# Performance work log

Measured on AMD Instinct MI355X. Metric: run time of the kernel, lower is better.

## Reference

```python
import jax, jax.numpy as jnp
import numpy as np
import math

B, S, D, H = 4, 2048, 1024, 16
DK = D // H

def setup_inputs() -> dict:
    key = jax.random.key(0)
    ks = jax.random.split(key, 6)
    scale = 1.0 / math.sqrt(D)
    x = jax.random.normal(ks[0], (B, S, D), dtype=jnp.float32)
    mask = jnp.tril(jnp.ones((S, S), dtype=jnp.int32))[None, None]  # [1,1,S,S] causal
    Wq = jax.random.normal(ks[1], (D, D), dtype=jnp.float32) * scale
    Wk = jax.random.normal(ks[2], (D, D), dtype=jnp.float32) * scale
    Wv = jax.random.normal(ks[3], (D, D), dtype=jnp.float32) * scale
    Wo = jax.random.normal(ks[4], (D, D), dtype=jnp.float32) * scale
    z = jnp.zeros((D,), dtype=jnp.float32)
    return {"x": x, "mask": mask, "Wq": Wq, "bq": z, "Wk": Wk, "bk": z,
            "Wv": Wv, "bv": z, "Wo": Wo, "bo": z}

def reference(x, mask, Wq, bq, Wk, bk, Wv, bv, Wo, bo):
    bsz, seq_len, d_model = x.shape
    def split_heads(t):  # [B,S,D] -> [B,H,S,DK]
        return t.reshape(bsz, seq_len, H, DK).transpose(0, 2, 1, 3)
    Q = split_heads(x @ Wq + bq)
    K = split_heads(x @ Wk + bk)
    V = split_heads(x @ Wv + bv)
    scores = jnp.einsum('bhqd,bhkd->bhqk', Q, K) / jnp.sqrt(jnp.asarray(DK, x.dtype))
    scores = jnp.where(mask == 0, jnp.asarray(-jnp.inf, x.dtype), scores)
    attn = jax.nn.softmax(scores, axis=-1)
    # dropout is identity in eval mode
    context = jnp.einsum('bhqk,bhkd->bhqd', attn, V)
    context = context.transpose(0, 2, 1, 3).reshape(bsz, seq_len, d_model)
    return context @ Wo + bo
```

## Files before the change

### kernel.cpp

```cpp
#include <hip/hip_runtime.h>
#include <hip/hip_bf16.h>
#include <math.h>

#define BATCH 4
#define SEQ   2048
#define DMODEL 1024
#define NHEAD 16
#define DHEAD 64
#define MROWS (BATCH * SEQ)
#define SC_Q  0.1803368801111244f

typedef __attribute__((ext_vector_type(8))) short short8;
typedef __attribute__((ext_vector_type(4))) float f32x4;
typedef __attribute__((ext_vector_type(4))) unsigned short ushort4v;

__device__ inline unsigned short f2bf(float f) {
    union { float f; unsigned int u; } v; v.f = f;
    unsigned int r = v.u + 0x7FFFu + ((v.u >> 16) & 1u);
    return (unsigned short)(r >> 16);
}

__device__ inline unsigned int cvt_pk_bf16(float a, float b) {
    unsigned int r;
    asm("v_cvt_pk_bf16_f32 %0, %1, %2" : "=v"(r) : "v"(a), "v"(b));
    return r;
}

__device__ __forceinline__ void g2l16(const unsigned short* g, unsigned short* l) {
    __builtin_amdgcn_global_load_lds(
        (const __attribute__((address_space(1))) unsigned int*)g,
        (__attribute__((address_space(3))) unsigned int*)l, 16, 0, 0);
}

#define SBAR()  do { __builtin_amdgcn_s_barrier(); asm volatile("" ::: "memory"); } while (0)

__global__ __launch_bounds__(256) void cvt_bf16_kernel(
    const float* __restrict__ src, unsigned short* __restrict__ dst, int n4)
{
    const int i = blockIdx.x * 256 + threadIdx.x;
    if (i < n4) {
        float4 v = ((const float4*)src)[i];
        ushort4v o = { f2bf(v.x), f2bf(v.y), f2bf(v.z), f2bf(v.w) };
        ((ushort4v*)dst)[i] = o;
    }
}

__global__ __launch_bounds__(256) void bias_pack_kernel(
    const float* __restrict__ bq, const float* __restrict__ bk,
    const float* __restrict__ bv, float* __restrict__ b3)
{
    const int i = blockIdx.x * 256 + threadIdx.x;
    if (i < DMODEL) {
        b3[i]              = bq[i];
        b3[i + DMODEL]     = bk[i];
        b3[i + 2 * DMODEL] = bv[i];
    }
}

__global__ __launch_bounds__(256) void transpose_cvt_kernel(
    const float* __restrict__ W0, const float* __restrict__ W1,
    const float* __restrict__ W2, const float* __restrict__ W3,
    unsigned short* __restrict__ T0, unsigned short* __restrict__ T1,
    unsigned short* __restrict__ T2, unsigned short* __restrict__ T3)
{
    const float* W; unsigned short* T;
    switch (blockIdx.z) {
        case 0: W = W0; T = T0; break;
        case 1: W = W1; T = T1; break;
        case 2: W = W2; T = T2; break;
        default: W = W3; T = T3; break;
    }
    __shared__ float tile[32][33];
    const int r0 = blockIdx.y * 32, c0 = blockIdx.x * 32;
    const int c = threadIdx.x & 31, r = threadIdx.x >> 5;
    #pragma unroll
    for (int i = 0; i < 4; ++i)
        tile[r + i * 8][c] = W[(size_t)(r0 + r + i * 8) * DMODEL + c0 + c];
    __syncthreads();
    #pragma unroll
    for (int i = 0; i < 4; ++i)
        T[(size_t)(c0 + r + i * 8) * DMODEL + r0 + c] = f2bf(tile[c][r + i * 8]);
}

__global__ __launch_bounds__(256) void transpose_v_kernel(
    const unsigned short* __restrict__ Vin, unsigned short* __restrict__ Vt)
{
    __shared__ unsigned short t[64][72];
    const int tid = threadIdx.x;
    const int kt = blockIdx.x, bh = blockIdx.y;
    const unsigned short* src = Vin + ((size_t)bh * SEQ + kt * 64) * DHEAD;
    const int r = tid >> 3, c = (tid & 7) * 8;
    *(short8*)&t[r][c]      = *(const short8*)(src + (size_t)r * DHEAD + c);
    *(short8*)&t[r + 32][c] = *(const short8*)(src + (size_t)(r + 32) * DHEAD + c);
    __syncthreads();
    unsigned short* dst = Vt + (size_t)bh * DHEAD * SEQ + kt * 64;
    const int d = tid >> 3, p0 = (tid & 7) * 8;
    short8 v0, v1;
    #pragma unroll
    for (int i = 0; i < 8; ++i) {
        const int p = p0 + i;
        const int k = (p & 32) | (((p >> 2) & 1) << 4) | (((p >> 3) & 3) << 2) | (p & 3);
        v0[i] = (short)t[k][d];
        v1[i] = (short)t[k][d + 32];
    }
    *(short8*)(dst + (size_t)d * SEQ + p0)        = v0;
    *(short8*)(dst + (size_t)(d + 32) * SEQ + p0) = v1;
}

__device__ __forceinline__ void gemm_main_8ph(
    const unsigned short* __restrict__ A, const unsigned short* __restrict__ Bt,
    f32x4 (&acc)[4][4], int m0, int n0, int wm, int wn, int l15, int quad)
{
    __shared__ unsigned short As[3][256 * 64];
    __shared__ unsigned short Bs[3][128 * 64];

    const int tid = threadIdx.x;

    #pragma unroll
    for (int i = 0; i < 4; ++i)
        #pragma unroll
        for (int j = 0; j < 4; ++j) acc[i][j] = (f32x4){0.f, 0.f, 0.f, 0.f};

    const unsigned short* gA[4];
    const unsigned short* gB[2];
    int cA[4], cB[2];
    #pragma unroll
    for (int j = 0; j < 4; ++j) {
        const int c = tid + j * 512, row = c >> 3, gq = (c & 7) ^ (row & 7);
        gA[j] = A + (size_t)(m0 + row) * DMODEL + gq * 8;
        cA[j] = c * 8;
    }
    #pragma unroll
    for (int j = 0; j < 2; ++j) {
        const int c = tid + j * 512, row = c >> 3, gq = (c & 7) ^ (row & 7);
        gB[j] = Bt + (size_t)(n0 + row) * DMODEL + gq * 8;
        cB[j] = c * 8;
    }

    #pragma unroll
    for (int tt = 0; tt < 2; ++tt) {
        #pragma unroll
        for (int j = 0; j < 4; ++j) { g2l16(gA[j], &As[tt][cA[j]]); gA[j] += 64; }
        #pragma unroll
        for (int j = 0; j < 2; ++j) { g2l16(gB[j], &Bs[tt][cB[j]]); gB[j] += 64; }
    }
    asm volatile("s_waitcnt vmcnt(6)" ::: "memory");
    SBAR();

    const int rm[4] = { wm + l15, wm + 16 + l15, wm + 32 + l15, wm + 48 + l15 };
    const int rn[4] = { wn + l15, wn + 16 + l15, wn + 32 + l15, wn + 48 + l15 };

    int cur = 0, sb = 2;
    #pragma unroll 1
    for (int t = 0; t < DMODEL / 64; ++t) {
        const unsigned short* As_c = &As[cur][0];
        const unsigned short* Bs_c = &Bs[cur][0];
        unsigned short* As_s = &As[sb][0];
        unsigned short* Bs_s = &Bs[sb][0];
        const bool st = (t < DMODEL / 64 - 2);

        short8 af[4], bfr[4];

        #pragma unroll
        for (int i = 0; i < 4; ++i) {
            af[i]  = *(const short8*)&As_c[rm[i] * 64 + (quad ^ (rm[i] & 7)) * 8];
            bfr[i] = *(const short8*)&Bs_c[rn[i] * 64 + (quad ^ (rn[i] & 7)) * 8];
        }
        if (st) { g2l16(gA[0], &As_s[cA[0]]); gA[0] += 64;
                  g2l16(gA[1], &As_s[cA[1]]); gA[1] += 64;
                  g2l16(gA[2], &As_s[cA[2]]); gA[2] += 64; }
        SBAR();
        __builtin_amdgcn_s_setprio(1);
        #pragma unroll
        for (int mi = 0; mi < 4; ++mi)
            #pragma unroll
            for (int ni = 0; ni < 4; ++ni)
                acc[mi][ni] = __builtin_amdgcn_mfma_f32_16x16x32_bf16(
                    af[mi], bfr[ni], acc[mi][ni], 0, 0, 0);
        __builtin_amdgcn_s_setprio(0);
        SBAR();

        #pragma unroll
        for (int i = 0; i < 4; ++i) {
            af[i]  = *(const short8*)&As_c[rm[i] * 64 + ((4 + quad) ^ (rm[i] & 7)) * 8];
            bfr[i] = *(const short8*)&Bs_c[rn[i] * 64 + ((4 + quad) ^ (rn[i] & 7)) * 8];
        }
        if (st) { g2l16(gA[3], &As_s[cA[3]]); gA[3] += 64;
                  g2l16(gB[0], &Bs_s[cB[0]]); gB[0] += 64;
                  g2l16(gB[1], &Bs_s[cB[1]]); gB[1] += 64; }
        if (st)
            asm volatile("s_waitcnt vmcnt(6)" ::: "memory");
        else if (t == DMODEL / 64 - 2)
            asm volatile("s_waitcnt vmcnt(0)" ::: "memory");
        SBAR();
        __builtin_amdgcn_s_setprio(1);
        #pragma unroll
        for (int mi = 0; mi < 4; ++mi)
            #pragma unroll
            for (int ni = 0; ni < 4; ++ni)
                acc[mi][ni] = __builtin_amdgcn_mfma_f32_16x16x32_bf16(
                    af[mi], bfr[ni], acc[mi][ni], 0, 0, 0);
        __builtin_amdgcn_s_setprio(0);
        SBAR();

        cur = (cur == 2) ? 0 : cur + 1;
        sb  = (sb  == 2) ? 0 : sb  + 1;
    }
}

__global__ __launch_bounds__(512, 2) void gemm_qkv(
    const unsigned short* __restrict__ A, const unsigned short* __restrict__ Bt,
    const float* __restrict__ bias3, unsigned short* __restrict__ QKV )
{
    const int tid  = threadIdx.x;
    const int wave = tid >> 6, lane = tid & 63;
    const int l15  = lane & 15, quad = lane >> 4;
    const int wm   = (wave >> 1) * 64;
    const int wn   = (wave & 1) * 64;
    const int m0   = blockIdx.y * 256;
    const int n0   = blockIdx.x * 128;

    f32x4 acc[4][4];
    gemm_main_8ph(A, Bt, acc, m0, n0, wm, wn, l15, quad);

    const size_t elems = (size_t)MROWS * DMODEL;
    #pragma unroll
    for (int mi = 0; mi < 4; ++mi) {
        #pragma unroll
        for (int r = 0; r < 4; ++r) {
            const int m = m0 + wm + mi * 16 + quad * 4 + r;
            const int b = m >> 11, s = m & 2047;
            #pragma unroll
            for (int ni = 0; ni < 4; ++ni) {
                const int n   = n0 + wn + ni * 16 + l15;
                const int seg = n >> 10, nn = n & 1023;
                const int h = nn >> 6, dk = nn & 63;
                const float sc  = (seg == 0) ? SC_Q : 1.0f;
                const float val = (acc[mi][ni][r] + bias3[n]) * sc;
                QKV[seg * elems + (((size_t)(b * NHEAD + h)) * SEQ + s) * DHEAD + dk] = f2bf(val);
            }
        }
    }
}

__global__ __launch_bounds__(512, 2) void gemm_out(
    const unsigned short* __restrict__ A, const unsigned short* __restrict__ Bt,
    const float* __restrict__ bias, float* __restrict__ Cout)
{
    const int tid  = threadIdx.x;
    const int wave = tid >> 6, lane = tid & 63;
    const int l15  = lane & 15, quad = lane >> 4;
    const int wm   = (wave >> 1) * 64;
    const int wn   = (wave & 1) * 64;
    const int m0   = blockIdx.y * 256;
    const int n0   = blockIdx.x * 128;

    f32x4 acc[4][4];
    gemm_main_8ph(A, Bt, acc, m0, n0, wm, wn, l15, quad);

    #pragma unroll
    for (int mi = 0; mi < 4; ++mi) {
        #pragma unroll
        for (int r = 0; r < 4; ++r) {
            const int m = m0 + wm + mi * 16 + quad * 4 + r;
            #pragma unroll
            for (int ni = 0; ni < 4; ++ni) {
                const int n = n0 + wn + ni * 16 + l15;
                Cout[(size_t)m * DMODEL + n] = acc[mi][ni][r] + bias[n];
            }
        }
    }
}

__global__ __launch_bounds__(256, 4) void attn_mfma7(
    const unsigned short* __restrict__ Q, const unsigned short* __restrict__ K,
    const unsigned short* __restrict__ VtG, unsigned short* __restrict__ ctx_out)
{
    __shared__ alignas(16) unsigned short Ks[2][64 * 64];
    __shared__ alignas(16) unsigned short Vs[2][64 * 64];

    const int tid  = threadIdx.x;
    const int wave = tid >> 6, lane = tid & 63;
    const int l15  = lane & 15, quad = lane >> 4;
    const int qa   = blockIdx.x;
    const int qb   = 31 - qa;
    const int bh   = blockIdx.y;
    const int b    = bh >> 4, h = bh & 15;

    const unsigned short* Kb0 = K   + (size_t)bh * SEQ * DHEAD;
    const unsigned short* Vb0 = VtG + (size_t)bh * DHEAD * SEQ;

    short8 qf[2][2];
    #pragma unroll
    for (int g = 0; g < 2; ++g) {
        const int qtile = g ? qb : qa;
        const unsigned short* qrow =
            Q + ((size_t)bh * SEQ + qtile * 64 + wave * 16 + l15) * DHEAD + quad * 8;
        qf[g][0] = *(const short8*)qrow;
        qf[g][1] = *(const short8*)(qrow + 32);
    }

    f32x4 Of[2][4];
    float lsum[2] = {0.f, 0.f};
    #pragma unroll
    for (int g = 0; g < 2; ++g)
        #pragma unroll
        for (int i = 0; i < 4; ++i) Of[g][i] = (f32x4){0.f, 0.f, 0.f, 0.f};

    const int qloc = wave * 16 + l15;
    const f32x4 zero4 = (f32x4){0.f, 0.f, 0.f, 0.f};

    const int ck0 = tid >> 3, cg0 = tid & 7;
    const int ck1 = (tid + 256) >> 3, cg1 = tid & 7;

    #define STAGE(buf, jb)                                                          \
        do {                                                                        \
            const unsigned short* Kt_ = Kb0 + (size_t)(jb) * 64 * DHEAD;            \
            const unsigned short* Vt_ = Vb0 + (jb) * 64;                            \
            g2l16(Kt_ + (size_t)ck0 * DHEAD + (cg0 ^ (ck0 & 7)) * 8,                \
                  &Ks[buf][(tid) * 8]);                                             \
            g2l16(Vt_ + (size_t)ck0 * SEQ   + (cg0 ^ (ck0 & 7)) * 8,                \
                  &Vs[buf][(tid) * 8]);                                             \
            g2l16(Kt_ + (size_t)ck1 * DHEAD + (cg1 ^ (ck1 & 7)) * 8,                \
                  &Ks[buf][(tid + 256) * 8]);                                       \
            g2l16(Vt_ + (size_t)ck1 * SEQ   + (cg1 ^ (ck1 & 7)) * 8,                \
                  &Vs[buf][(tid + 256) * 8]);                                       \
        } while (0)

    STAGE(0, 0);

    for (int jb = 0; jb <= qb; ++jb) {
        const int cur = jb & 1;
        asm volatile("s_waitcnt vmcnt(0)" ::: "memory");
        __syncthreads();
        if (jb < qb) STAGE(cur ^ 1, jb + 1);

        const bool act0  = (jb <= qa);
        const bool diag0 = (jb == qa);
        const bool diag1 = (jb == qb);
        const unsigned short* KsC = &Ks[cur][0];
        const unsigned short* VsC = &Vs[cur][0];

        union { unsigned int u[4]; short8 v; } pa[2][2];
        #pragma unroll
        for (int nt = 0; nt < 4; ++nt) {
            const int k = nt * 16 + l15;
            const short8 a0 = *(const short8*)&KsC[(k * 8 + ( quad      ^ (k & 7))) * 8];
            const short8 a1 = *(const short8*)&KsC[(k * 8 + ((quad + 4) ^ (k & 7))) * 8];

            f32x4 s1 = __builtin_amdgcn_mfma_f32_16x16x32_bf16(a0, qf[1][0], zero4, 0, 0, 0);
            s1       = __builtin_amdgcn_mfma_f32_16x16x32_bf16(a1, qf[1][1], s1,    0, 0, 0);
            f32x4 p1;
            #pragma unroll
            for (int r = 0; r < 4; ++r) p1[r] = __builtin_amdgcn_exp2f(s1[r]);
            if (diag1) {
                #pragma unroll
                for (int r = 0; r < 4; ++r)
                    if (nt * 16 + quad * 4 + r > qloc) p1[r] = 0.f;
            }
            lsum[1] += (p1[0] + p1[1]) + (p1[2] + p1[3]);
            pa[1][nt >> 1].u[(nt & 1) * 2]     = cvt_pk_bf16(p1[0], p1[1]);
            pa[1][nt >> 1].u[(nt & 1) * 2 + 1] = cvt_pk_bf16(p1[2], p1[3]);

            if (act0) {
                f32x4 s0 = __builtin_amdgcn_mfma_f32_16x16x32_bf16(a0, qf[0][0], zero4, 0, 0, 0);
                s0       = __builtin_amdgcn_mfma_f32_16x16x32_bf16(a1, qf[0][1], s0,    0, 0, 0);
                f32x4 p0;
                #pragma unroll
                for (int r = 0; r < 4; ++r) p0[r] = __builtin_amdgcn_exp2f(s0[r]);
                if (diag0) {
                    #pragma unroll
                    for (int r = 0; r < 4; ++r)
                        if (nt * 16 + quad * 4 + r > qloc) p0[r] = 0.f;
                }
                lsum[0] += (p0[0] + p0[1]) + (p0[2] + p0[3]);
                pa[0][nt >> 1].u[(nt & 1) * 2]     = cvt_pk_bf16(p0[0], p0[1]);
                pa[0][nt >> 1].u[(nt & 1) * 2 + 1] = cvt_pk_bf16(p0[2], p0[3]);
            }
        }

        #pragma unroll
        for (int cc = 0; cc < 2; ++cc) {
            #pragma unroll
            for (int nt = 0; nt < 4; ++nt) {
                const int d = nt * 16 + l15;
                const short8 vb = *(const short8*)
                    &VsC[(d * 8 + ((cc * 4 + quad) ^ (d & 7))) * 8];
                Of[1][nt] = __builtin_amdgcn_mfma_f32_16x16x32_bf16(
                    pa[1][cc].v, vb, Of[1][nt], 0, 0, 0);
                if (act0)
                    Of[0][nt] = __builtin_amdgcn_mfma_f32_16x16x32_bf16(
                        pa[0][cc].v, vb, Of[0][nt], 0, 0, 0);
            }
        }
    }
    #undef STAGE

    #pragma unroll
    for (int g = 0; g < 2; ++g) {
        const int qtile = g ? qb : qa;
        float l = lsum[g];
        l += __shfl_xor(l, 16);
        l += __shfl_xor(l, 32);
        #pragma unroll
        for (int r = 0; r < 4; ++r) {
            const float inv = 1.0f / __shfl(l, quad * 4 + r);
            const int s = qtile * 64 + wave * 16 + quad * 4 + r;
            unsigned short* o = ctx_out + ((size_t)(b * SEQ + s)) * DMODEL + h * DHEAD;
            #pragma unroll
            for (int nt = 0; nt < 4; ++nt)
                o[nt * 16 + l15] = f2bf(Of[g][nt][r] * inv);
        }
    }
}

extern "C" void kernel_launch(void* const* d_in, const int* in_sizes, int n_in,
                              void* d_out, int out_size, void* d_ws, size_t ws_size,
                              hipStream_t stream) {
    const float* x  = (const float*)d_in[0];
    const float* Wq = (const float*)d_in[2];
    const float* bq = (const float*)d_in[3];
    const float* Wk = (const float*)d_in[4];
    const float* bk = (const float*)d_in[5];
    const float* Wv = (const float*)d_in[6];
    const float* bv = (const float*)d_in[7];
    const float* Wo = (const float*)d_in[8];
    const float* bo = (const float*)d_in[9];
    float* out = (float*)d_out;

    const size_t elems  = (size_t)MROWS * DMODEL;
    const size_t welems = (size_t)DMODEL * DMODEL;
    unsigned short* xbf   = (unsigned short*)d_ws;
    unsigned short* WqkvT = xbf + elems;
    unsigned short* WoT   = WqkvT + 3 * welems;
    unsigned short* Qbuf  = WoT + welems;
    unsigned short* Kbuf  = Qbuf + elems;
    unsigned short* Vbuf  = Kbuf + elems;
    unsigned short* VtG   = Vbuf + elems;
    unsigned short* Cbuf  = VtG + elems;
    float*          bias3 = (float*)(Cbuf + elems);

    dim3 blk(256);
    dim3 blk2(512);

    cvt_bf16_kernel<<<dim3((int)(elems / 4 / 256)), blk, 0, stream>>>(x, xbf, (int)(elems / 4));
    transpose_cvt_kernel<<<dim3(32, 32, 4), blk, 0, stream>>>(
        Wq, Wk, Wv, Wo, WqkvT, WqkvT + welems, WqkvT + 2 * welems, WoT);
    bias_pack_kernel<<<dim3(4), blk, 0, stream>>>(bq, bk, bv, bias3);

    dim3 gqkv(3 * DMODEL / 128, MROWS / 256);
    gemm_qkv<<<gqkv, blk2, 0, stream>>>(xbf, WqkvT, bias3, Qbuf);

    transpose_v_kernel<<<dim3(SEQ / 64, BATCH * NHEAD), blk, 0, stream>>>(Vbuf, VtG);

    dim3 gattn(16, BATCH * NHEAD);
    attn_mfma7<<<gattn, blk, 0, stream>>>(Qbuf, Kbuf, VtG, Cbuf);

    dim3 gout(DMODEL / 128, MROWS / 256);
    gemm_out<<<gout, blk2, 0, stream>>>(Cbuf, WoT, bo, out);
}
```

Before: 275.9 us.

## Merge prep kernels into one launch and add wave priority hints in attention

The three preprocessing kernels (x bf16 conversion, weight transpose-convert, bias packing) become one launch that dispatches on block index, removing two kernel launches and the gaps between them. In the attention loop, s_setprio raises wave priority around the MFMA/exp sections, and __syncthreads is replaced by a raw s_barrier with a compiler memory fence. The merged kernel has divergent block roles and a shared-memory tile that only the transpose branch uses. The priority hints may or may not improve interleaving between the waves on a SIMD.

```diff
diff --git a/kernel.cpp b/kernel.cpp
--- a/kernel.cpp
+++ b/kernel.cpp
@@ -34,52 +34,51 @@
 
 #define SBAR()  do { __builtin_amdgcn_s_barrier(); asm volatile("" ::: "memory"); } while (0)
 
-__global__ __launch_bounds__(256) void cvt_bf16_kernel(
-    const float* __restrict__ src, unsigned short* __restrict__ dst, int n4)
-{
-    const int i = blockIdx.x * 256 + threadIdx.x;
-    if (i < n4) {
-        float4 v = ((const float4*)src)[i];
-        ushort4v o = { f2bf(v.x), f2bf(v.y), f2bf(v.z), f2bf(v.w) };
-        ((ushort4v*)dst)[i] = o;
-    }
-}
-
-__global__ __launch_bounds__(256) void bias_pack_kernel(
-    const float* __restrict__ bq, const float* __restrict__ bk,
-    const float* __restrict__ bv, float* __restrict__ b3)
-{
-    const int i = blockIdx.x * 256 + threadIdx.x;
-    if (i < DMODEL) {
-        b3[i]              = bq[i];
-        b3[i + DMODEL]     = bk[i];
-        b3[i + 2 * DMODEL] = bv[i];
-    }
-}
-
-__global__ __launch_bounds__(256) void transpose_cvt_kernel(
+__global__ __launch_bounds__(256) void prep_kernel(
+    const float* __restrict__ x, unsigned short* __restrict__ xbf,
     const float* __restrict__ W0, const float* __restrict__ W1,
     const float* __restrict__ W2, const float* __restrict__ W3,
     unsigned short* __restrict__ T0, unsigned short* __restrict__ T1,
-    unsigned short* __restrict__ T2, unsigned short* __restrict__ T3)
-{
-    const float* W; unsigned short* T;
-    switch (blockIdx.z) {
-        case 0: W = W0; T = T0; break;
-        case 1: W = W1; T = T1; break;
-        case 2: W = W2; T = T2; break;
-        default: W = W3; T = T3; break;
-    }
+    unsigned short* __restrict__ T2, unsigned short* __restrict__ T3,
+    const float* __restrict__ bq, const float* __restrict__ bk,
+    const float* __restrict__ bv, float* __restrict__ b3)
+{
     __shared__ float tile[32][33];
-    const int r0 = blockIdx.y * 32, c0 = blockIdx.x * 32;
-    const int c = threadIdx.x & 31, r = threadIdx.x >> 5;
-    #pragma unroll
-    for (int i = 0; i < 4; ++i)
-        tile[r + i * 8][c] = W[(size_t)(r0 + r + i * 8) * DMODEL + c0 + c];
-    __syncthreads();
-    #pragma unroll
-    for (int i = 0; i < 4; ++i)
-        T[(size_t)(c0 + r + i * 8) * DMODEL + r0 + c] = f2bf(tile[c][r + i * 8]);
+    const int bid = blockIdx.x, tid = threadIdx.x;
+
+    if (bid < 8192) {
+        const int i = bid * 256 + tid;
+        float4 v = ((const float4*)x)[i];
+        ushort4v o = { f2bf(v.x), f2bf(v.y), f2bf(v.z), f2bf(v.w) };
+        ((ushort4v*)xbf)[i] = o;
+    } else if (bid < 12288) {
+        const int t = bid - 8192;
+        const int z = t >> 10, rem = t & 1023;
+        const int by = rem >> 5, bx = rem & 31;
+        const float* W; unsigned short* T;
+        switch (z) {
+            case 0: W = W0; T = T0; break;
+            case 1: W = W1; T = T1; break;
+            case 2: W = W2; T = T2; break;
+            default: W = W3; T = T3; break;
+        }
+        const int r0 = by * 32, c0 = bx * 32;
+        const int c = tid & 31, r = tid >> 5;
+        #pragma unroll
+        for (int i = 0; i < 4; ++i)
+            tile[r + i * 8][c] = W[(size_t)(r0 + r + i * 8) * DMODEL + c0 + c];
+        __syncthreads();
+        #pragma unroll
+        for (int i = 0; i < 4; ++i)
+            T[(size_t)(c0 + r + i * 8) * DMODEL + r0 + c] = f2bf(tile[c][r + i * 8]);
+    } else {
+        const int i = (bid - 12288) * 256 + tid;
+        if (i < DMODEL) {
+            b3[i]              = bq[i];
+            b3[i + DMODEL]     = bk[i];
+            b3[i + 2 * DMODEL] = bv[i];
+        }
+    }
 }
 
 __global__ __launch_bounds__(256) void transpose_v_kernel(
@@ -272,7 +271,7 @@
     }
 }
 
-__global__ __launch_bounds__(256, 4) void attn_mfma7(
+__global__ __launch_bounds__(256, 4) void attn_mfma8(
     const unsigned short* __restrict__ Q, const unsigned short* __restrict__ K,
     const unsigned short* __restrict__ VtG, unsigned short* __restrict__ ctx_out)
 {
@@ -332,7 +331,7 @@
     for (int jb = 0; jb <= qb; ++jb) {
         const int cur = jb & 1;
         asm volatile("s_waitcnt vmcnt(0)" ::: "memory");
-        __syncthreads();
+        SBAR();
         if (jb < qb) STAGE(cur ^ 1, jb + 1);
 
         const bool act0  = (jb <= qa);
@@ -342,6 +341,7 @@
         const unsigned short* VsC = &Vs[cur][0];
 
         union { unsigned int u[4]; short8 v; } pa[2][2];
+        __builtin_amdgcn_s_setprio(1);
         #pragma unroll
         for (int nt = 0; nt < 4; ++nt) {
             const int k = nt * 16 + l15;
@@ -378,7 +378,9 @@
                 pa[0][nt >> 1].u[(nt & 1) * 2 + 1] = cvt_pk_bf16(p0[2], p0[3]);
             }
         }
-
+        __builtin_amdgcn_s_setprio(0);
+
+        __builtin_amdgcn_s_setprio(1);
         #pragma unroll
         for (int cc = 0; cc < 2; ++cc) {
             #pragma unroll
@@ -393,6 +395,7 @@
                         pa[0][cc].v, vb, Of[0][nt], 0, 0, 0);
             }
         }
+        __builtin_amdgcn_s_setprio(0);
     }
     #undef STAGE
 
@@ -443,10 +446,10 @@
     dim3 blk(256);
     dim3 blk2(512);
 
-    cvt_bf16_kernel<<<dim3((int)(elems / 4 / 256)), blk, 0, stream>>>(x, xbf, (int)(elems / 4));
-    transpose_cvt_kernel<<<dim3(32, 32, 4), blk, 0, stream>>>(
-        Wq, Wk, Wv, Wo, WqkvT, WqkvT + welems, WqkvT + 2 * welems, WoT);
-    bias_pack_kernel<<<dim3(4), blk, 0, stream>>>(bq, bk, bv, bias3);
+    prep_kernel<<<dim3(12292), blk, 0, stream>>>(
+        x, xbf, Wq, Wk, Wv, Wo,
+        WqkvT, WqkvT + welems, WqkvT + 2 * welems, WoT,
+        bq, bk, bv, bias3);
 
     dim3 gqkv(3 * DMODEL / 128, MROWS / 256);
     gemm_qkv<<<gqkv, blk2, 0, stream>>>(xbf, WqkvT, bias3, Qbuf);
@@ -454,7 +457,7 @@
     transpose_v_kernel<<<dim3(SEQ / 64, BATCH * NHEAD), blk, 0, stream>>>(Vbuf, VtG);
 
     dim3 gattn(16, BATCH * NHEAD);
-    attn_mfma7<<<gattn, blk, 0, stream>>>(Qbuf, Kbuf, VtG, Cbuf);
+    attn_mfma8<<<gattn, blk, 0, stream>>>(Qbuf, Kbuf, VtG, Cbuf);
 
     dim3 gout(DMODEL / 128, MROWS / 256);
     gemm_out<<<gout, blk2, 0, stream>>>(Cbuf, WoT, bo, out);
```

New measurement: 275.3 us. About the same (-0.2%).
